# Optimization experiments

Measured on AMD Instinct MI355X. Metric: run time of the kernel, lower is better.

## Reference

```python
import jax, jax.numpy as jnp
import numpy as np

H = 1024      # hidden_dim
NH = 16       # num_heads
HD = H // NH  # head_dim
EPS = 1e-12
SCALE = float(np.sqrt(H))


def setup_inputs() -> dict:
    key = jax.random.key(0)
    ks = jax.random.split(key, 12)
    S, B = 2048, 2
    inp = {
        "query": jax.random.normal(ks[0], (S, B, 2 * H), jnp.float32),
        "key":   jax.random.normal(ks[1], (S, B, H), jnp.float32),
        "value": jax.random.normal(ks[2], (S, B, H), jnp.float32),
        # gating params (zeros in torch init, but randomize for a meaningful test)
        "qs": jax.random.normal(ks[3], (1, 1, H), jnp.float32) * 0.02,
        "ks_p": jax.random.normal(ks[4], (1, 1, H), jnp.float32) * 0.02,
        "vs": jax.random.normal(ks[5], (1, 1, H), jnp.float32) * 0.02,
        # Overparam vq: Linear(H, 2H)
        "vq_w": jax.random.normal(ks[6], (2 * H, H), jnp.float32) * (1.0 / np.sqrt(H)),
        "vq_b": jax.random.normal(ks[7], (2 * H,), jnp.float32) * 0.02,
        # q_linear: Linear(2H, H)
        "ql_w": jax.random.normal(ks[8], (H, 2 * H), jnp.float32) * (1.0 / np.sqrt(2 * H)),
        "ql_b": jax.random.normal(ks[9], (H,), jnp.float32) * 0.02,
        # LayerNorm(H)
        "ln_g": jnp.ones((H,), jnp.float32),
        "ln_b": jnp.zeros((H,), jnp.float32),
    }
    return inp


def _layernorm(x, g, b):
    mu = jnp.mean(x, axis=-1, keepdims=True)
    var = jnp.mean(jnp.square(x - mu), axis=-1, keepdims=True)
    return (x - mu) * jax.lax.rsqrt(var + EPS) * g + b


def reference(query, key, value, qs, ks_p, vs, vq_w, vq_b, ql_w, ql_b, ln_g, ln_b):
    # gate vectors
    qsig = jax.nn.sigmoid(qs)            # [1,1,H]
    ksig = jax.nn.sigmoid(ks_p)          # [1,1,H]
    # vq = Overparam(sigmoid(vs)): c,f = l1(x).split(H); sigmoid(f)*tanh(c)
    h = jax.nn.sigmoid(vs) @ vq_w.T + vq_b   # [1,1,2H]
    c, f = h[..., :H], h[..., H:]
    vsig = jax.nn.sigmoid(f) * jnp.tanh(c)   # [1,1,H]

    q = qsig * _layernorm(query @ ql_w.T + ql_b, ln_g, ln_b)  # [S,B,H]
    k = ksig * key
    v = vsig * value

    # batch-first
    q = jnp.transpose(q, (1, 0, 2))  # [B,Q,H]
    k = jnp.transpose(k, (1, 0, 2))  # [B,K,H]
    v = jnp.transpose(v, (1, 0, 2))
    B, Q, _ = q.shape
    K = k.shape[1]

    qh = q.reshape(B, Q, NH, HD)
    kh = k.reshape(B, K, NH, HD)
    vh = v.reshape(B, K, NH, HD)

    scores = jnp.einsum('bqhd,bkhd->bhqk', qh, kh) / SCALE
    w = jax.nn.softmax(scores, axis=-1)                # [B,NH,Q,K]
    out = jnp.einsum('bhqk,bkhd->bqhd', w, vh).reshape(B, Q, H)
    # torch code's final .transpose(0,1) is not assigned -> output is [Q,B,H]
    return jnp.transpose(out, (1, 0, 2))
```

## Files before the change

kernel.cpp:

```cpp
#include <hip/hip_runtime.h>

typedef __bf16 bf16x8 __attribute__((ext_vector_type(8)));
typedef float f32x4 __attribute__((ext_vector_type(4)));
typedef unsigned short u16x8 __attribute__((ext_vector_type(8)));
typedef unsigned short u16x4 __attribute__((ext_vector_type(4)));
typedef unsigned short u16;
typedef unsigned int u32;


#define LOG2E 1.4426950408889634f

__device__ __forceinline__ float b2f(u16 u) {
  union { unsigned int i; float f; } x; x.i = ((unsigned int)u) << 16; return x.f;
}
__device__ __forceinline__ u16 f2b(float f) {
  union { float f; unsigned int i; } x; x.f = f;
  unsigned int r = (x.i + 0x7fffu + ((x.i >> 16) & 1u)) >> 16;
  return (u16)r;
}
__device__ __forceinline__ float sigm(float x) { return 1.0f / (1.0f + __expf(-x)); }

__device__ __forceinline__ void async16(u16* lds, const u16* g) {
  __builtin_amdgcn_global_load_lds((const __attribute__((address_space(1))) void*)g,
                                   (__attribute__((address_space(3))) void*)lds, 16, 0, 0);
}

__global__ __launch_bounds__(256) void k_cvt_all(const float4* __restrict__ q, u16x4* __restrict__ qd,
                                                 const float4* __restrict__ w, u16x4* __restrict__ wd,
                                                 const float4* __restrict__ k, u16x4* __restrict__ kd,
                                                 const float4* __restrict__ v, u16x4* __restrict__ vd) {
  int b = blockIdx.x;
  const float4* s; u16x4* d; int i;
  if (b < 8192)       { s = q; d = qd; i = b * 256 + threadIdx.x; }
  else if (b < 10240) { s = w; d = wd; i = (b - 8192) * 256 + threadIdx.x; }
  else if (b < 14336) { s = k; d = kd; i = (b - 10240) * 256 + threadIdx.x; }
  else                { s = v; d = vd; i = (b - 14336) * 256 + threadIdx.x; }
  float4 x = s[i];
  u16x4 o; o[0] = f2b(x.x); o[1] = f2b(x.y); o[2] = f2b(x.z); o[3] = f2b(x.w);
  d[i] = o;
}

__global__ __launch_bounds__(256) void k_h(const float* __restrict__ vs,
                                           const float* __restrict__ vq_w,
                                           const float* __restrict__ vq_b,
                                           float* __restrict__ h) {
  __shared__ float svs[1024];
  int t = threadIdx.x;
  for (int i = t; i < 1024; i += 256) svs[i] = sigm(vs[i]);
  __syncthreads();
  int wave = t >> 6, lane = t & 63;
  int row = blockIdx.x * 4 + wave;
  const float4* w4 = (const float4*)(vq_w + (size_t)row * 1024);
  const float4* s4 = (const float4*)svs;
  float acc = 0.f;
#pragma unroll
  for (int k = 0; k < 4; ++k) {
    float4 w = w4[k * 64 + lane];
    float4 s = s4[k * 64 + lane];
    acc += w.x * s.x + w.y * s.y + w.z * s.z + w.w * s.w;
  }
#pragma unroll
  for (int off = 1; off < 64; off <<= 1) acc += __shfl_xor(acc, off);
  if (lane == 0) h[row] = acc + vq_b[row];
}

__global__ __launch_bounds__(256) void k_gemm(const u16* __restrict__ A,
                                              const u16* __restrict__ Bt,
                                              u16* __restrict__ C) {
  __shared__ __align__(16) u16 As[128 * 32];
  __shared__ __align__(16) u16 Bs[128 * 32];
  int tid = threadIdx.x;
  int wave = tid >> 6, lane = tid & 63;
  int l15 = lane & 15, quad = lane >> 4;
  int bx = blockIdx.x & 255;
  int kh = blockIdx.x >> 8;
  int kofs = kh << 10;
  int m0 = (bx >> 3) * 128;
  int n0 = (bx & 7) * 128;
  int wm = (wave >> 1) * 64, wn = (wave & 1) * 64;
  f32x4 acc[4][4] = {};
  int c1 = tid, c2 = tid + 256;
  const u16* ga1 = A + (size_t)(m0 + (c1 >> 2)) * 2048 + kofs + (c1 & 3) * 8;
  const u16* ga2 = A + (size_t)(m0 + (c2 >> 2)) * 2048 + kofs + (c2 & 3) * 8;
  const u16* gb1 = Bt + (size_t)(n0 + (c1 >> 2)) * 2048 + kofs + (c1 & 3) * 8;
  const u16* gb2 = Bt + (size_t)(n0 + (c2 >> 2)) * 2048 + kofs + (c2 & 3) * 8;
  u16* lA1 = As + wave * 512;
  u16* lA2 = As + 2048 + wave * 512;
  u16* lB1 = Bs + wave * 512;
  u16* lB2 = Bs + 2048 + wave * 512;
  for (int kt = 0; kt < 32; ++kt) {
    async16(lA1, ga1); async16(lA2, ga2);
    async16(lB1, gb1); async16(lB2, gb2);
    ga1 += 32; ga2 += 32; gb1 += 32; gb2 += 32;
    __syncthreads();
    bf16x8 af[4], bfr[4];
#pragma unroll
    for (int mt = 0; mt < 4; ++mt)
      af[mt] = *(const bf16x8*)(As + (wm + mt * 16 + l15) * 32 + quad * 8);
#pragma unroll
    for (int nt = 0; nt < 4; ++nt)
      bfr[nt] = *(const bf16x8*)(Bs + (wn + nt * 16 + l15) * 32 + quad * 8);
#pragma unroll
    for (int mt = 0; mt < 4; ++mt)
#pragma unroll
      for (int nt = 0; nt < 4; ++nt)
        acc[mt][nt] = __builtin_amdgcn_mfma_f32_16x16x32_bf16(af[mt], bfr[nt], acc[mt][nt], 0, 0, 0);
    __syncthreads();
  }
  u16* Cp = C + (size_t)kh * 4096 * 1024;
#pragma unroll
  for (int mt = 0; mt < 4; ++mt) {
#pragma unroll
    for (int r = 0; r < 4; ++r) {
      int m = m0 + wm + mt * 16 + quad * 4 + r;
      u16* crow = Cp + (size_t)m * 1024 + n0 + wn + l15;
#pragma unroll
      for (int nt = 0; nt < 4; ++nt) crow[nt * 16] = f2b(acc[mt][nt][r]);
    }
  }
}

__global__ __launch_bounds__(256) void k_ln(const u16* __restrict__ qpre0,
                                            const u16* __restrict__ qpre1,
                                            const float* __restrict__ ql_b,
                                            const float* __restrict__ ln_g,
                                            const float* __restrict__ ln_b,
                                            const float* __restrict__ qs,
                                            const float* __restrict__ ks,
                                            u16* __restrict__ qatt) {
  int row = blockIdx.x;
  int t = threadIdx.x;
  u16x4 a4 = *(const u16x4*)(qpre0 + (size_t)row * 1024 + t * 4);
  u16x4 b4 = *(const u16x4*)(qpre1 + (size_t)row * 1024 + t * 4);
  float v[4];
  float s = 0.f, ss = 0.f;
#pragma unroll
  for (int j = 0; j < 4; ++j) {
    v[j] = b2f(a4[j]) + b2f(b4[j]) + ql_b[t * 4 + j];
    s += v[j]; ss += v[j] * v[j];
  }
#pragma unroll
  for (int off = 1; off < 64; off <<= 1) { s += __shfl_xor(s, off); ss += __shfl_xor(ss, off); }
  __shared__ float red[8];
  int wv = t >> 6, ln = t & 63;
  if (ln == 0) { red[wv] = s; red[4 + wv] = ss; }
  __syncthreads();
  s = red[0] + red[1] + red[2] + red[3];
  ss = red[4] + red[5] + red[6] + red[7];
  float mu = s * (1.f / 1024.f);
  float rstd = rsqrtf(ss * (1.f / 1024.f) - mu * mu + 1e-12f);
  int sidx = row >> 1, b = row & 1;
  int ch0 = t * 4;
  int hh = ch0 >> 6, hd0 = ch0 & 63;
  u16* dst = qatt + ((size_t)(b * 16 + hh) * 2048 + sidx) * 64 + hd0;
#pragma unroll
  for (int j = 0; j < 4; ++j) {
    int ch = ch0 + j;
    float gate = sigm(qs[ch]) * sigm(ks[ch]) * (LOG2E / 32.0f);
    float y = (v[j] - mu) * rstd * ln_g[ch] + ln_b[ch];
    dst[j] = f2b(y * gate);
  }
}

__global__ __launch_bounds__(256, 2) void k_attn(const u16* __restrict__ qatt,
                                                 const u16* __restrict__ key,
                                                 const u16* __restrict__ value,
                                                 const float* __restrict__ hbuf,
                                                 float* __restrict__ out) {
  int bh = blockIdx.x & 31;
  int qt = blockIdx.x >> 5;
  int b = bh >> 4, h = bh & 15;
  int tid = threadIdx.x, wave = tid >> 6, lane = tid & 63;
  int l15 = lane & 15, quad = lane >> 4;
  int q0 = qt * 128;

  __shared__ __align__(16) u16 Kt[2][64 * 72];
  __shared__ __align__(16) u16 Vt[2][64 * 72];
  __shared__ __align__(16) u16 Pb[4][32 * 72];

  bf16x8 qf[2][2];
#pragma unroll
  for (int f = 0; f < 2; ++f) {
    const u16* qrow = qatt + ((size_t)bh * 2048 + q0 + f * 64 + wave * 16 + l15) * 64 + quad * 8;
    qf[f][0] = *(const bf16x8*)qrow;
    qf[f][1] = *(const bf16x8*)(qrow + 32);
  }

  const u16* kb = key + (size_t)b * 1024 + (size_t)h * 64;
  const u16* vb = value + (size_t)b * 1024 + (size_t)h * 64;
  u16* Pw = Pb[wave];

  int p = lane & 31;
  int chbase = wave * 16 + (lane >> 5) * 8;
  const u16* vsrc = vb + (size_t)2 * p * 2048 + chbase;
  int krow = wave * 16 + (lane >> 3);
  int kch  = (lane & 7) * 8;
  const u16* ksrc = kb + (size_t)krow * 2048 + kch;
  int kdofs = krow * 72 + kch;
  int vdofs_base = 2 * p;

  {
    u16x8 k0 = *(const u16x8*)ksrc;
    u16x8 k1 = *(const u16x8*)(ksrc + (size_t)8 * 2048);
    *(u16x8*)(&Kt[0][kdofs]) = k0;
    *(u16x8*)(&Kt[0][kdofs + 8 * 72]) = k1;
    u16x8 va = *(const u16x8*)vsrc;
    u16x8 vbq = *(const u16x8*)(vsrc + 2048);
#pragma unroll
    for (int c = 0; c < 8; ++c) {
      u32 pk = (u32)va[c] | ((u32)vbq[c] << 16);
      *(u32*)(&Vt[0][(chbase + c) * 72 + vdofs_base]) = pk;
    }
  }
  __syncthreads();

  f32x4 oacc[2][4] = {};
  float l_i[2][4] = {};

  for (int kt = 0; kt < 32; ++kt) {
    int cur = kt & 1;
    f32x4 sacc[2][4] = {};
    const u16* ktc = Kt[cur];
#pragma unroll
    for (int nt = 0; nt < 4; ++nt) {
      const u16* kr = ktc + (nt * 16 + l15) * 72 + quad * 8;
      bf16x8 kfa = *(const bf16x8*)kr;
      bf16x8 kfb = *(const bf16x8*)(kr + 32);
      sacc[0][nt] = __builtin_amdgcn_mfma_f32_16x16x32_bf16(qf[0][0], kfa, sacc[0][nt], 0, 0, 0);
      sacc[0][nt] = __builtin_amdgcn_mfma_f32_16x16x32_bf16(qf[0][1], kfb, sacc[0][nt], 0, 0, 0);
      sacc[1][nt] = __builtin_amdgcn_mfma_f32_16x16x32_bf16(qf[1][0], kfa, sacc[1][nt], 0, 0, 0);
      sacc[1][nt] = __builtin_amdgcn_mfma_f32_16x16x32_bf16(qf[1][1], kfb, sacc[1][nt], 0, 0, 0);
    }
    u16x8 pk0, pk1, va, vbq;
    if (kt < 31) {
      const u16* ks2 = ksrc + (size_t)(kt + 1) * 64 * 2048;
      pk0 = *(const u16x8*)ks2;
      pk1 = *(const u16x8*)(ks2 + (size_t)8 * 2048);
      const u16* vs2 = vsrc + (size_t)(kt + 1) * 64 * 2048;
      va = *(const u16x8*)vs2;
      vbq = *(const u16x8*)(vs2 + 2048);
    }
#pragma unroll
    for (int f = 0; f < 2; ++f) {
#pragma unroll
      for (int r = 0; r < 4; ++r) {
        float p0 = __builtin_amdgcn_exp2f(sacc[f][0][r]);
        float p1 = __builtin_amdgcn_exp2f(sacc[f][1][r]);
        float p2 = __builtin_amdgcn_exp2f(sacc[f][2][r]);
        float p3 = __builtin_amdgcn_exp2f(sacc[f][3][r]);
        l_i[f][r] += (p0 + p1) + (p2 + p3);
        u16* prow = Pw + (f * 16 + quad * 4 + r) * 72 + l15;
        prow[0]  = f2b(p0);
        prow[16] = f2b(p1);
        prow[32] = f2b(p2);
        prow[48] = f2b(p3);
      }
    }
    bf16x8 pf[2][2];
#pragma unroll
    for (int f = 0; f < 2; ++f) {
      pf[f][0] = *(const bf16x8*)(Pw + (f * 16 + l15) * 72 + quad * 8);
      pf[f][1] = *(const bf16x8*)(Pw + (f * 16 + l15) * 72 + 32 + quad * 8);
    }
    const u16* vt = Vt[cur];
#pragma unroll
    for (int nt = 0; nt < 4; ++nt) {
      const u16* vr = vt + (nt * 16 + l15) * 72 + quad * 8;
      bf16x8 vf0 = *(const bf16x8*)vr;
      bf16x8 vf1 = *(const bf16x8*)(vr + 32);
      oacc[0][nt] = __builtin_amdgcn_mfma_f32_16x16x32_bf16(pf[0][0], vf0, oacc[0][nt], 0, 0, 0);
      oacc[0][nt] = __builtin_amdgcn_mfma_f32_16x16x32_bf16(pf[0][1], vf1, oacc[0][nt], 0, 0, 0);
      oacc[1][nt] = __builtin_amdgcn_mfma_f32_16x16x32_bf16(pf[1][0], vf0, oacc[1][nt], 0, 0, 0);
      oacc[1][nt] = __builtin_amdgcn_mfma_f32_16x16x32_bf16(pf[1][1], vf1, oacc[1][nt], 0, 0, 0);
    }
    if (kt < 31) {
      u16* kd = Kt[cur ^ 1];
      *(u16x8*)(&kd[kdofs]) = pk0;
      *(u16x8*)(&kd[kdofs + 8 * 72]) = pk1;
      u16* vd = Vt[cur ^ 1];
#pragma unroll
      for (int c = 0; c < 8; ++c) {
        u32 pk = (u32)va[c] | ((u32)vbq[c] << 16);
        *(u32*)(&vd[(chbase + c) * 72 + vdofs_base]) = pk;
      }
    }
    __syncthreads();
  }
#pragma unroll
  for (int f = 0; f < 2; ++f)
#pragma unroll
    for (int r = 0; r < 4; ++r) {
      float l = l_i[f][r];
      l += __shfl_xor(l, 1);
      l += __shfl_xor(l, 2);
      l += __shfl_xor(l, 4);
      l += __shfl_xor(l, 8);
      l_i[f][r] = l;
    }
  float vsg[4];
#pragma unroll
  for (int nt = 0; nt < 4; ++nt) {
    int ch = h * 64 + nt * 16 + l15;
    vsg[nt] = sigm(hbuf[1024 + ch]) * tanhf(hbuf[ch]);
  }
#pragma unroll
  for (int f = 0; f < 2; ++f)
#pragma unroll
    for (int r = 0; r < 4; ++r) {
      int sq = q0 + f * 64 + wave * 16 + quad * 4 + r;
      float inv = 1.0f / l_i[f][r];
      float* orow = out + ((size_t)sq * 2 + b) * 1024 + h * 64;
#pragma unroll
      for (int nt = 0; nt < 4; ++nt)
        orow[nt * 16 + l15] = oacc[f][nt][r] * inv * vsg[nt];
    }
}

extern "C" void kernel_launch(void* const* d_in, const int* in_sizes, int n_in,
                              void* d_out, int out_size, void* d_ws, size_t ws_size,
                              hipStream_t stream) {
  (void)in_sizes; (void)n_in; (void)out_size; (void)ws_size;
  const float* query = (const float*)d_in[0];
  const float* key   = (const float*)d_in[1];
  const float* value = (const float*)d_in[2];
  const float* qs    = (const float*)d_in[3];
  const float* ksp   = (const float*)d_in[4];
  const float* vs    = (const float*)d_in[5];
  const float* vq_w  = (const float*)d_in[6];
  const float* vq_b  = (const float*)d_in[7];
  const float* ql_w  = (const float*)d_in[8];
  const float* ql_b  = (const float*)d_in[9];
  const float* ln_g  = (const float*)d_in[10];
  const float* ln_b  = (const float*)d_in[11];
  float* out = (float*)d_out;

  float* ws = (float*)d_ws;
  float* h   = ws;
  u16* qpre  = (u16*)(ws + 4096);
  u16* qbf   = qpre + (size_t)2 * 4096 * 1024;
  u16* qatt  = qbf;
  u16* wbf   = qbf + (size_t)4096 * 2048;
  u16* kbf   = wbf + (size_t)1024 * 2048;
  u16* vbf   = kbf + (size_t)4096 * 1024;

  hipLaunchKernelGGL(k_cvt_all, dim3(18432), dim3(256), 0, stream,
                     (const float4*)query, (u16x4*)qbf,
                     (const float4*)ql_w,  (u16x4*)wbf,
                     (const float4*)key,   (u16x4*)kbf,
                     (const float4*)value, (u16x4*)vbf);
  hipLaunchKernelGGL(k_h,    dim3(512),  dim3(256), 0, stream, vs, vq_w, vq_b, h);
  hipLaunchKernelGGL(k_gemm, dim3(512),  dim3(256), 0, stream, qbf, wbf, qpre);
  hipLaunchKernelGGL(k_ln,   dim3(4096), dim3(256), 0, stream, qpre, qpre + (size_t)4096 * 1024,
                     ql_b, ln_g, ln_b, qs, ksp, qatt);
  hipLaunchKernelGGL(k_attn, dim3(512),  dim3(256), 0, stream, qatt, kbf, vbf, h, out);
}
```

Before: 244.4 us.

## Compute transposed scores so P stays in registers; load K directly to registers

The score MFMA now takes K as the A operand and Q as B, so the score tile comes out transposed. Each lane then already holds the exp values it needs as the A operand of the PV MFMA, and they are packed with v_cvt_pk_bf16_f32 without going through LDS. K fragments are loaded straight from global memory into double-buffered registers, which removes the K tile in LDS. V is stored in an unpadded LDS layout with XOR swizzling, and the row-sum reduction is changed to match the new layout. This cuts LDS traffic and footprint, but raises register pressure, and each lane now issues more scattered global loads for K.

Result: slower. 258.4 us (+5.7%).

```diff
diff --git a/kernel.cpp b/kernel.cpp
--- a/kernel.cpp
+++ b/kernel.cpp
@@ -19,6 +19,9 @@
   return (u16)r;
 }
 __device__ __forceinline__ float sigm(float x) { return 1.0f / (1.0f + __expf(-x)); }
+__device__ __forceinline__ u32 cvtpk(float lo, float hi) {
+  u32 r; asm("v_cvt_pk_bf16_f32 %0, %1, %2" : "=v"(r) : "v"(lo), "v"(hi)); return r;
+}
 
 __device__ __forceinline__ void async16(u16* lds, const u16* g) {
   __builtin_amdgcn_global_load_lds((const __attribute__((address_space(1))) void*)g,
@@ -162,6 +165,86 @@
   }
 }
 
+__device__ __forceinline__ f32x4 mfma16(bf16x8 a, bf16x8 b, f32x4 c) {
+  return __builtin_amdgcn_mfma_f32_16x16x32_bf16(a, b, c, 0, 0, 0);
+}
+
+template <int CUR>
+__device__ __forceinline__ void attn_iter(bool pref,
+                                          bf16x8 (&kC)[4][2], bf16x8 (&kN)[4][2],
+                                          const bf16x8 (&qf)[2][2],
+                                          const u16* (&kp)[4], const u16*& vp,
+                                          u16 (&Vt)[2][64 * 64],
+                                          f32x4 (&oacc)[2][4], float (&l_i)[2],
+                                          int chbase, int pcol, int l15, int colA, int colB) {
+  f32x4 sacc[2][4] = {};
+#pragma unroll
+  for (int nt = 0; nt < 4; ++nt) {
+    bf16x8 k0 = kC[nt][0], k1 = kC[nt][1];
+    sacc[0][nt] = mfma16(k0, qf[0][0], sacc[0][nt]);
+    sacc[0][nt] = mfma16(k1, qf[0][1], sacc[0][nt]);
+    sacc[1][nt] = mfma16(k0, qf[1][0], sacc[1][nt]);
+    sacc[1][nt] = mfma16(k1, qf[1][1], sacc[1][nt]);
+  }
+  u16x8 va, vq;
+  if (pref) {
+#pragma unroll
+    for (int nt = 0; nt < 4; ++nt) {
+      kp[nt] += 64 * 2048;
+      kN[nt][0] = *(const bf16x8*)kp[nt];
+      kN[nt][1] = *(const bf16x8*)(kp[nt] + 32);
+    }
+    vp += 64 * 2048;
+    va = *(const u16x8*)vp;
+    vq = *(const u16x8*)(vp + 2048);
+  }
+  u32 pw[2][8];
+#pragma unroll
+  for (int f = 0; f < 2; ++f) {
+    float pe[4][4];
+    float ls = 0.f;
+#pragma unroll
+    for (int nt = 0; nt < 4; ++nt) {
+#pragma unroll
+      for (int r = 0; r < 4; ++r) pe[nt][r] = __builtin_amdgcn_exp2f(sacc[f][nt][r]);
+      ls += (pe[nt][0] + pe[nt][1]) + (pe[nt][2] + pe[nt][3]);
+    }
+    l_i[f] += ls;
+    pw[f][0] = cvtpk(pe[0][0], pe[0][1]); pw[f][1] = cvtpk(pe[0][2], pe[0][3]);
+    pw[f][2] = cvtpk(pe[1][0], pe[1][1]); pw[f][3] = cvtpk(pe[1][2], pe[1][3]);
+    pw[f][4] = cvtpk(pe[2][0], pe[2][1]); pw[f][5] = cvtpk(pe[2][2], pe[2][3]);
+    pw[f][6] = cvtpk(pe[3][0], pe[3][1]); pw[f][7] = cvtpk(pe[3][2], pe[3][3]);
+  }
+  union U8 { u32 w[4]; bf16x8 v; };
+  bf16x8 pa[2][2];
+#pragma unroll
+  for (int f = 0; f < 2; ++f) {
+    U8 t0; t0.w[0] = pw[f][0]; t0.w[1] = pw[f][1]; t0.w[2] = pw[f][2]; t0.w[3] = pw[f][3];
+    U8 t1; t1.w[0] = pw[f][4]; t1.w[1] = pw[f][5]; t1.w[2] = pw[f][6]; t1.w[3] = pw[f][7];
+    pa[f][0] = t0.v; pa[f][1] = t1.v;
+  }
+  const u16* vt0 = Vt[CUR];
+#pragma unroll
+  for (int nt = 0; nt < 4; ++nt) {
+    const u16* vrow = vt0 + (nt * 16 + l15) * 64;
+    bf16x8 vA = *(const bf16x8*)(vrow + colA);
+    bf16x8 vB = *(const bf16x8*)(vrow + colB);
+    oacc[0][nt] = mfma16(pa[0][0], vA, oacc[0][nt]);
+    oacc[0][nt] = mfma16(pa[0][1], vB, oacc[0][nt]);
+    oacc[1][nt] = mfma16(pa[1][0], vA, oacc[1][nt]);
+    oacc[1][nt] = mfma16(pa[1][1], vB, oacc[1][nt]);
+  }
+  if (pref) {
+    u16* vd = (u16*)Vt[CUR ^ 1];
+#pragma unroll
+    for (int c = 0; c < 8; ++c) {
+      u32 pk2 = (u32)va[c] | ((u32)vq[c] << 16);
+      *(u32*)&vd[(chbase + c) * 64 + (pcol ^ (c << 3))] = pk2;
+    }
+  }
+  __syncthreads();
+}
+
 __global__ __launch_bounds__(256, 2) void k_attn(const u16* __restrict__ qatt,
                                                  const u16* __restrict__ key,
                                                  const u16* __restrict__ value,
@@ -174,9 +257,7 @@
   int l15 = lane & 15, quad = lane >> 4;
   int q0 = qt * 128;
 
-  __shared__ __align__(16) u16 Kt[2][64 * 72];
-  __shared__ __align__(16) u16 Vt[2][64 * 72];
-  __shared__ __align__(16) u16 Pb[4][32 * 72];
+  __shared__ __align__(16) u16 Vt[2][64 * 64];
 
   bf16x8 qf[2][2];
 #pragma unroll
@@ -188,115 +269,52 @@
 
   const u16* kb = key + (size_t)b * 1024 + (size_t)h * 64;
   const u16* vb = value + (size_t)b * 1024 + (size_t)h * 64;
-  u16* Pw = Pb[wave];
+
+  const u16* kp[4];
+#pragma unroll
+  for (int nt = 0; nt < 4; ++nt) kp[nt] = kb + (size_t)(nt * 16 + l15) * 2048 + quad * 8;
 
   int p = lane & 31;
   int chbase = wave * 16 + (lane >> 5) * 8;
-  const u16* vsrc = vb + (size_t)2 * p * 2048 + chbase;
-  int krow = wave * 16 + (lane >> 3);
-  int kch  = (lane & 7) * 8;
-  const u16* ksrc = kb + (size_t)krow * 2048 + kch;
-  int kdofs = krow * 72 + kch;
-  int vdofs_base = 2 * p;
-
+  const u16* vp = vb + (size_t)2 * p * 2048 + chbase;
+  int kk = 2 * p;
+  int pcol = ((kk >> 5) & 1) * 32 + ((kk >> 2) & 3) * 8 + ((kk >> 4) & 1) * 4 + (kk & 3);
+  int swr = (l15 & 7) << 3;
+  int colA = (8 * quad) ^ swr;
+  int colB = (32 + 8 * quad) ^ swr;
+
+  bf16x8 kA[4][2], kB[4][2];
+#pragma unroll
+  for (int nt = 0; nt < 4; ++nt) {
+    kA[nt][0] = *(const bf16x8*)kp[nt];
+    kA[nt][1] = *(const bf16x8*)(kp[nt] + 32);
+  }
   {
-    u16x8 k0 = *(const u16x8*)ksrc;
-    u16x8 k1 = *(const u16x8*)(ksrc + (size_t)8 * 2048);
-    *(u16x8*)(&Kt[0][kdofs]) = k0;
-    *(u16x8*)(&Kt[0][kdofs + 8 * 72]) = k1;
-    u16x8 va = *(const u16x8*)vsrc;
-    u16x8 vbq = *(const u16x8*)(vsrc + 2048);
+    u16x8 va = *(const u16x8*)vp;
+    u16x8 vq = *(const u16x8*)(vp + 2048);
 #pragma unroll
     for (int c = 0; c < 8; ++c) {
-      u32 pk = (u32)va[c] | ((u32)vbq[c] << 16);
-      *(u32*)(&Vt[0][(chbase + c) * 72 + vdofs_base]) = pk;
+      u32 pk2 = (u32)va[c] | ((u32)vq[c] << 16);
+      *(u32*)&Vt[0][(chbase + c) * 64 + (pcol ^ (c << 3))] = pk2;
     }
   }
   __syncthreads();
 
   f32x4 oacc[2][4] = {};
-  float l_i[2][4] = {};
-
-  for (int kt = 0; kt < 32; ++kt) {
-    int cur = kt & 1;
-    f32x4 sacc[2][4] = {};
-    const u16* ktc = Kt[cur];
-#pragma unroll
-    for (int nt = 0; nt < 4; ++nt) {
-      const u16* kr = ktc + (nt * 16 + l15) * 72 + quad * 8;
-      bf16x8 kfa = *(const bf16x8*)kr;
-      bf16x8 kfb = *(const bf16x8*)(kr + 32);
-      sacc[0][nt] = __builtin_amdgcn_mfma_f32_16x16x32_bf16(qf[0][0], kfa, sacc[0][nt], 0, 0, 0);
-      sacc[0][nt] = __builtin_amdgcn_mfma_f32_16x16x32_bf16(qf[0][1], kfb, sacc[0][nt], 0, 0, 0);
-      sacc[1][nt] = __builtin_amdgcn_mfma_f32_16x16x32_bf16(qf[1][0], kfa, sacc[1][nt], 0, 0, 0);
-      sacc[1][nt] = __builtin_amdgcn_mfma_f32_16x16x32_bf16(qf[1][1], kfb, sacc[1][nt], 0, 0, 0);
-    }
-    u16x8 pk0, pk1, va, vbq;
-    if (kt < 31) {
-      const u16* ks2 = ksrc + (size_t)(kt + 1) * 64 * 2048;
-      pk0 = *(const u16x8*)ks2;
-      pk1 = *(const u16x8*)(ks2 + (size_t)8 * 2048);
-      const u16* vs2 = vsrc + (size_t)(kt + 1) * 64 * 2048;
-      va = *(const u16x8*)vs2;
-      vbq = *(const u16x8*)(vs2 + 2048);
-    }
-#pragma unroll
-    for (int f = 0; f < 2; ++f) {
-#pragma unroll
-      for (int r = 0; r < 4; ++r) {
-        float p0 = __builtin_amdgcn_exp2f(sacc[f][0][r]);
-        float p1 = __builtin_amdgcn_exp2f(sacc[f][1][r]);
-        float p2 = __builtin_amdgcn_exp2f(sacc[f][2][r]);
-        float p3 = __builtin_amdgcn_exp2f(sacc[f][3][r]);
-        l_i[f][r] += (p0 + p1) + (p2 + p3);
-        u16* prow = Pw + (f * 16 + quad * 4 + r) * 72 + l15;
-        prow[0]  = f2b(p0);
-        prow[16] = f2b(p1);
-        prow[32] = f2b(p2);
-        prow[48] = f2b(p3);
-      }
-    }
-    bf16x8 pf[2][2];
-#pragma unroll
-    for (int f = 0; f < 2; ++f) {
-      pf[f][0] = *(const bf16x8*)(Pw + (f * 16 + l15) * 72 + quad * 8);
-      pf[f][1] = *(const bf16x8*)(Pw + (f * 16 + l15) * 72 + 32 + quad * 8);
-    }
-    const u16* vt = Vt[cur];
-#pragma unroll
-    for (int nt = 0; nt < 4; ++nt) {
-      const u16* vr = vt + (nt * 16 + l15) * 72 + quad * 8;
-      bf16x8 vf0 = *(const bf16x8*)vr;
-      bf16x8 vf1 = *(const bf16x8*)(vr + 32);
-      oacc[0][nt] = __builtin_amdgcn_mfma_f32_16x16x32_bf16(pf[0][0], vf0, oacc[0][nt], 0, 0, 0);
-      oacc[0][nt] = __builtin_amdgcn_mfma_f32_16x16x32_bf16(pf[0][1], vf1, oacc[0][nt], 0, 0, 0);
-      oacc[1][nt] = __builtin_amdgcn_mfma_f32_16x16x32_bf16(pf[1][0], vf0, oacc[1][nt], 0, 0, 0);
-      oacc[1][nt] = __builtin_amdgcn_mfma_f32_16x16x32_bf16(pf[1][1], vf1, oacc[1][nt], 0, 0, 0);
-    }
-    if (kt < 31) {
-      u16* kd = Kt[cur ^ 1];
-      *(u16x8*)(&kd[kdofs]) = pk0;
-      *(u16x8*)(&kd[kdofs + 8 * 72]) = pk1;
-      u16* vd = Vt[cur ^ 1];
-#pragma unroll
-      for (int c = 0; c < 8; ++c) {
-        u32 pk = (u32)va[c] | ((u32)vbq[c] << 16);
-        *(u32*)(&vd[(chbase + c) * 72 + vdofs_base]) = pk;
-      }
-    }
-    __syncthreads();
-  }
-#pragma unroll
-  for (int f = 0; f < 2; ++f)
-#pragma unroll
-    for (int r = 0; r < 4; ++r) {
-      float l = l_i[f][r];
-      l += __shfl_xor(l, 1);
-      l += __shfl_xor(l, 2);
-      l += __shfl_xor(l, 4);
-      l += __shfl_xor(l, 8);
-      l_i[f][r] = l;
-    }
+  float l_i[2] = {};
+
+  for (int kt = 0; kt < 32; kt += 2) {
+    attn_iter<0>(true, kA, kB, qf, kp, vp, Vt, oacc, l_i, chbase, pcol, l15, colA, colB);
+    attn_iter<1>(kt < 30, kB, kA, qf, kp, vp, Vt, oacc, l_i, chbase, pcol, l15, colA, colB);
+  }
+
+#pragma unroll
+  for (int f = 0; f < 2; ++f) {
+    float l = l_i[f];
+    l += __shfl_xor(l, 16);
+    l += __shfl_xor(l, 32);
+    l_i[f] = l;
+  }
   float vsg[4];
 #pragma unroll
   for (int nt = 0; nt < 4; ++nt) {
@@ -308,7 +326,7 @@
 #pragma unroll
     for (int r = 0; r < 4; ++r) {
       int sq = q0 + f * 64 + wave * 16 + quad * 4 + r;
-      float inv = 1.0f / l_i[f][r];
+      float inv = 1.0f / __shfl(l_i[f], quad * 4 + r);
       float* orow = out + ((size_t)sq * 2 + b) * 1024 + h * 64;
 #pragma unroll
       for (int nt = 0; nt < 4; ++nt)
```
